# Optimization experiments

Measured on AMD Instinct MI355X. Metric: run time of the kernel, lower is better.

Reference implementation:

```python
import jax, jax.numpy as jnp
import numpy as np

SEQ, BATCH, EMBED = 2048, 4, 768
NUM_HEADS = 12
HEAD_DIM = EMBED // NUM_HEADS
SCALING = HEAD_DIM ** -0.5


def setup_inputs() -> dict:
    key = jax.random.key(0)
    ks = jax.random.split(key, 9)
    std = 0.02
    d = {"x": jax.random.normal(ks[0], (SEQ, BATCH, EMBED), dtype=jnp.float32)}
    for i, n in enumerate(["q", "k", "v", "out"]):
        d[f"W{n}"] = jax.random.normal(ks[1 + 2 * i], (EMBED, EMBED), dtype=jnp.float32) * std
        d[f"b{n}"] = jax.random.normal(ks[2 + 2 * i], (EMBED,), dtype=jnp.float32) * std
    return d


def reference(x, Wq, bq, Wk, bk, Wv, bv, Wout, bout):
    # x: [tgt_len, bsz, embed_dim] (fairseq seq-first layout per forward body)
    T, B, E = x.shape
    H, Dh = NUM_HEADS, HEAD_DIM

    q = (x @ Wq.T + bq) * SCALING          # [T, B, E]
    k = x @ Wk.T + bk
    v = x @ Wv.T + bv

    # view(T, B*H, Dh).transpose(0, 1) -> [B*H, T, Dh]
    q = q.reshape(T, B * H, Dh).transpose(1, 0, 2)
    k = k.reshape(T, B * H, Dh).transpose(1, 0, 2)
    v = v.reshape(T, B * H, Dh).transpose(1, 0, 2)

    # bmm: [B*H, T, T] attention scores (full O(T^2) matrix, as in the original)
    scores = jnp.einsum('bqd,bkd->bqk', q, k)
    # util_softmax with onnx_trace=True: softmax in float32, then cast back
    probs = jax.nn.softmax(scores.astype(jnp.float32), axis=-1).astype(scores.dtype)
    # dropout p=0.0 -> identity

    attn = jnp.einsum('bqk,bkd->bqd', probs, v)           # [B*H, T, Dh]
    attn = attn.transpose(1, 0, 2).reshape(T, B, E)       # [T, B, E]
    return attn @ Wout.T + bout
```

## Files before the change

kernel.cpp:

```cpp
#include <hip/hip_runtime.h>
#include <hip/hip_bf16.h>

#define SEQ 2048
#define BATCH 4
#define EMBED 768
#define NHEAD 12
#define HDIM 64
#define NROWS (SEQ*BATCH)
#define GH (BATCH*NHEAD)
#define KVBLK 64
#define KVHALF (SEQ/2)

typedef __bf16 bf16;
typedef __attribute__((ext_vector_type(4))) __bf16 bf16x4;
typedef __attribute__((ext_vector_type(8))) __bf16 bf16x8;
typedef __attribute__((ext_vector_type(4))) float f32x4;

#define LOG2E 1.44269504088896340736f

__global__ __launch_bounds__(256) void cvt_kernel(const float* __restrict__ in,
                                                  bf16* __restrict__ out, int n4) {
  int i = blockIdx.x * 256 + threadIdx.x;
  if (i >= n4) return;
  float4 v = reinterpret_cast<const float4*>(in)[i];
  bf16x4 o;
  o[0] = (bf16)v.x; o[1] = (bf16)v.y; o[2] = (bf16)v.z; o[3] = (bf16)v.w;
  reinterpret_cast<bf16x4*>(out)[i] = o;
}

__global__ __launch_bounds__(256) void cvt_w4(const float* __restrict__ Wq,
                                              const float* __restrict__ Wk,
                                              const float* __restrict__ Wv,
                                              const float* __restrict__ Wo,
                                              bf16* __restrict__ Wqkvb,
                                              bf16* __restrict__ Wob) {
  const int n4 = EMBED * EMBED / 4;
  int i = blockIdx.x * 256 + threadIdx.x;
  if (i >= n4) return;
  const float* src;
  bf16* dst;
  switch (blockIdx.y) {
    case 0: src = Wq; dst = Wqkvb; break;
    case 1: src = Wk; dst = Wqkvb + EMBED * EMBED; break;
    case 2: src = Wv; dst = Wqkvb + 2 * EMBED * EMBED; break;
    default: src = Wo; dst = Wob; break;
  }
  float4 v = reinterpret_cast<const float4*>(src)[i];
  bf16x4 o;
  o[0] = (bf16)v.x; o[1] = (bf16)v.y; o[2] = (bf16)v.z; o[3] = (bf16)v.w;
  reinterpret_cast<bf16x4*>(dst)[i] = o;
}

__global__ __launch_bounds__(256) void gemm_qkv(const bf16* __restrict__ A,
                                                const bf16* __restrict__ B,
                                                const float* __restrict__ bq,
                                                const float* __restrict__ bk,
                                                const float* __restrict__ bv,
                                                bf16* __restrict__ Qh,
                                                bf16* __restrict__ Kh,
                                                bf16* __restrict__ Vt) {
  constexpr int K = EMBED;
  __shared__ bf16 As[128 * 32];
  __shared__ bf16 Bs[128 * 32];
  const int tid = threadIdx.x;
  const int l = tid & 63;
  const int w = tid >> 6;
  const int row0 = blockIdx.x * 128;
  const int col0 = blockIdx.y * 128;
  const int wm = (w >> 1) * 64;
  const int wn = (w & 1) * 64;
  const int l15 = l & 15, l4 = l >> 4;

  f32x4 acc[4][4] = {};

  for (int k0 = 0; k0 < K; k0 += 32) {
#pragma unroll
    for (int i = 0; i < 2; ++i) {
      int c = tid + i * 256;
      int r = c >> 2, cc = c & 3;
      __builtin_amdgcn_global_load_lds(
          (const __attribute__((address_space(1))) void*)(A + (size_t)(row0 + r) * K + k0 + cc * 8),
          (__attribute__((address_space(3))) void*)(As + c * 8), 16, 0, 0);
    }
#pragma unroll
    for (int i = 0; i < 2; ++i) {
      int c = tid + i * 256;
      int r = c >> 2, cc = c & 3;
      __builtin_amdgcn_global_load_lds(
          (const __attribute__((address_space(1))) void*)(B + (size_t)(col0 + r) * K + k0 + cc * 8),
          (__attribute__((address_space(3))) void*)(Bs + c * 8), 16, 0, 0);
    }
    __syncthreads();

    bf16x8 af[4], bfr[4];
#pragma unroll
    for (int i = 0; i < 4; ++i)
      af[i] = *reinterpret_cast<const bf16x8*>(&As[(wm + i * 16 + l15) * 32 + l4 * 8]);
#pragma unroll
    for (int j = 0; j < 4; ++j)
      bfr[j] = *reinterpret_cast<const bf16x8*>(&Bs[(wn + j * 16 + l15) * 32 + l4 * 8]);
#pragma unroll
    for (int i = 0; i < 4; ++i)
#pragma unroll
      for (int j = 0; j < 4; ++j)
        acc[i][j] = __builtin_amdgcn_mfma_f32_16x16x32_bf16(af[i], bfr[j], acc[i][j], 0, 0, 0);
    __syncthreads();
  }

  const int sel = blockIdx.y / 6;
  const float* bias = sel == 0 ? bq : (sel == 1 ? bk : bv);
  const int colbase = col0 - sel * EMBED;
#pragma unroll
  for (int i = 0; i < 4; ++i) {
#pragma unroll
    for (int j = 0; j < 4; ++j) {
      int col = colbase + wn + j * 16 + l15;
      float bia = bias[col];
#pragma unroll
      for (int r = 0; r < 4; ++r) {
        int row = row0 + wm + i * 16 + l4 * 4 + r;
        float v = acc[i][j][r] + bia;
        int t = row >> 2, bb = row & 3;
        int hh = col >> 6, d = col & 63;
        int g = bb * NHEAD + hh;
        if (sel == 0)      Qh[((size_t)g * SEQ + t) * HDIM + d] = (bf16)(v * (0.125f * LOG2E));
        else if (sel == 1) Kh[((size_t)g * SEQ + t) * HDIM + d] = (bf16)v;
        else               Vt[((size_t)g * HDIM + d) * SEQ + t] = (bf16)v;
      }
    }
  }
}

__global__ __launch_bounds__(256) void gemm_out(const bf16* __restrict__ A,
                                                const bf16* __restrict__ B,
                                                const float* __restrict__ bias,
                                                float* __restrict__ outp) {
  constexpr int K = EMBED;
  __shared__ bf16 As[128 * 32];
  __shared__ bf16 Bs[128 * 32];
  const int tid = threadIdx.x;
  const int l = tid & 63;
  const int w = tid >> 6;
  const int row0 = blockIdx.x * 128;
  const int col0 = blockIdx.y * 128;
  const int wm = (w >> 1) * 64;
  const int wn = (w & 1) * 64;
  const int l15 = l & 15, l4 = l >> 4;

  f32x4 acc[4][4] = {};

  for (int k0 = 0; k0 < K; k0 += 32) {
#pragma unroll
    for (int i = 0; i < 2; ++i) {
      int c = tid + i * 256;
      int r = c >> 2, cc = c & 3;
      __builtin_amdgcn_global_load_lds(
          (const __attribute__((address_space(1))) void*)(A + (size_t)(row0 + r) * K + k0 + cc * 8),
          (__attribute__((address_space(3))) void*)(As + c * 8), 16, 0, 0);
    }
#pragma unroll
    for (int i = 0; i < 2; ++i) {
      int c = tid + i * 256;
      int r = c >> 2, cc = c & 3;
      __builtin_amdgcn_global_load_lds(
          (const __attribute__((address_space(1))) void*)(B + (size_t)(col0 + r) * K + k0 + cc * 8),
          (__attribute__((address_space(3))) void*)(Bs + c * 8), 16, 0, 0);
    }
    __syncthreads();

    bf16x8 af[4], bfr[4];
#pragma unroll
    for (int i = 0; i < 4; ++i)
      af[i] = *reinterpret_cast<const bf16x8*>(&As[(wm + i * 16 + l15) * 32 + l4 * 8]);
#pragma unroll
    for (int j = 0; j < 4; ++j)
      bfr[j] = *reinterpret_cast<const bf16x8*>(&Bs[(wn + j * 16 + l15) * 32 + l4 * 8]);
#pragma unroll
    for (int i = 0; i < 4; ++i)
#pragma unroll
      for (int j = 0; j < 4; ++j)
        acc[i][j] = __builtin_amdgcn_mfma_f32_16x16x32_bf16(af[i], bfr[j], acc[i][j], 0, 0, 0);
    __syncthreads();
  }

#pragma unroll
  for (int i = 0; i < 4; ++i) {
#pragma unroll
    for (int j = 0; j < 4; ++j) {
      int col = col0 + wn + j * 16 + l15;
      float bia = bias[col];
#pragma unroll
      for (int r = 0; r < 4; ++r) {
        int row = row0 + wm + i * 16 + l4 * 4 + r;
        outp[(size_t)row * EMBED + col] = acc[i][j][r] + bia;
      }
    }
  }
}

__global__ __launch_bounds__(256, 4) void attn_kernel(const bf16* __restrict__ Qh,
                                                      const bf16* __restrict__ Kh,
                                                      const bf16* __restrict__ Vt,
                                                      bf16* __restrict__ O0,
                                                      bf16* __restrict__ O1,
                                                      float* __restrict__ Sums) {
  const int g = blockIdx.x % GH;
  const int r2 = blockIdx.x / GH;
  const int half = r2 & 1;
  const int q0 = (r2 >> 1) * 128;
  const int kvbase = half * KVHALF;
  const int tid = threadIdx.x;
  const int w = tid >> 6, l = tid & 63;
  const int l15 = l & 15, l4 = l >> 4;
  const int qw = q0 + w * 32;

  __shared__ bf16 Ks[2][KVBLK * HDIM];
  __shared__ bf16 Vs[HDIM * KVBLK];
  __shared__ bf16 P_all[4][32 * 64];

  bf16* P = (bf16*)P_all[w];
  const bf16* Qp = Qh + (size_t)g * SEQ * HDIM;
  const bf16* Kp = Kh + (size_t)g * SEQ * HDIM;
  const bf16* Vp = Vt + (size_t)g * HDIM * SEQ;

#define STAGE_K(buf, kv0)                                                               \
  do {                                                                                  \
    _Pragma("unroll") for (int i = 0; i < 2; ++i) {                                     \
      int t = i * 256 + tid;                                                            \
      int r = t >> 3, c = t & 7;                                                        \
      __builtin_amdgcn_global_load_lds(                                                 \
          (const __attribute__((address_space(1))) void*)(Kp + (size_t)((kv0) + r) * HDIM + ((c ^ (r & 7)) * 8)), \
          (__attribute__((address_space(3))) void*)(&Ks[buf][t * 8]), 16, 0, 0);        \
    }                                                                                   \
  } while (0)

#define STAGE_V(kv0)                                                                    \
  do {                                                                                  \
    _Pragma("unroll") for (int i = 0; i < 2; ++i) {                                     \
      int t = i * 256 + tid;                                                            \
      int r = t >> 3, c = t & 7;                                                        \
      __builtin_amdgcn_global_load_lds(                                                 \
          (const __attribute__((address_space(1))) void*)(Vp + (size_t)r * SEQ + (kv0) + ((c ^ (r & 7)) * 8)), \
          (__attribute__((address_space(3))) void*)(&Vs[t * 8]), 16, 0, 0);             \
    }                                                                                   \
  } while (0)

  bf16x8 aq[2][2];
#pragma unroll
  for (int qf = 0; qf < 2; ++qf)
#pragma unroll
    for (int ks = 0; ks < 2; ++ks)
      aq[qf][ks] = *reinterpret_cast<const bf16x8*>(
          Qp + (size_t)(qw + qf * 16 + l15) * HDIM + ks * 32 + l4 * 8);

  bf16x8 vone;
#pragma unroll
  for (int i = 0; i < 8; ++i) vone[i] = (bf16)1.0f;

  f32x4 acco[2][4] = {};
  f32x4 accs[2] = {};

  STAGE_K(0, kvbase);
  __syncthreads();

  int cur = 0;
  for (int kv0 = kvbase; kv0 < kvbase + KVHALF; kv0 += KVBLK) {
    STAGE_V(kv0);
    STAGE_K(cur ^ 1, kvbase + (((kv0 - kvbase) + KVBLK) & (KVHALF - 1)));

    f32x4 s[2][4] = {};
#pragma unroll
    for (int kf = 0; kf < 4; ++kf) {
      int row = kf * 16 + l15;
#pragma unroll
      for (int ks = 0; ks < 2; ++ks) {
        bf16x8 bk = *reinterpret_cast<const bf16x8*>(
            &Ks[cur][row * 64 + (((ks * 4 + l4) ^ (row & 7)) * 8)]);
        __builtin_amdgcn_s_setprio(1);
        s[0][kf] = __builtin_amdgcn_mfma_f32_16x16x32_bf16(bk, aq[0][ks], s[0][kf], 0, 0, 0);
        s[1][kf] = __builtin_amdgcn_mfma_f32_16x16x32_bf16(bk, aq[1][ks], s[1][kf], 0, 0, 0);
        __builtin_amdgcn_s_setprio(0);
      }
    }

#pragma unroll
    for (int qf = 0; qf < 2; ++qf) {
      int prow = qf * 16 + l15;
#pragma unroll
      for (int kf = 0; kf < 4; ++kf) {
        float p0 = exp2f(s[qf][kf][0]);
        float p1 = exp2f(s[qf][kf][1]);
        float p2 = exp2f(s[qf][kf][2]);
        float p3 = exp2f(s[qf][kf][3]);
        bf16x4 pk;
        pk[0] = (bf16)p0; pk[1] = (bf16)p1; pk[2] = (bf16)p2; pk[3] = (bf16)p3;
        int chunk = (2 * kf + (l4 >> 1)) ^ (prow & 7);
        *reinterpret_cast<bf16x4*>(&P[prow * 64 + chunk * 8 + (l4 & 1) * 4]) = pk;
      }
    }

    asm volatile("s_waitcnt vmcnt(2)" ::: "memory");

#pragma unroll
    for (int ks = 0; ks < 2; ++ks) {
      bf16x8 ap[2];
#pragma unroll
      for (int qf = 0; qf < 2; ++qf) {
        int prow = qf * 16 + l15;
        int lc = ks * 4 + l4;
        ap[qf] = *reinterpret_cast<const bf16x8*>(P + prow * 64 + ((lc ^ (prow & 7)) << 3));
      }
#pragma unroll
      for (int df = 0; df < 4; ++df) {
        int row = df * 16 + l15;
        bf16x8 bv = *reinterpret_cast<const bf16x8*>(
            &Vs[row * 64 + (((ks * 4 + l4) ^ (row & 7)) * 8)]);
        __builtin_amdgcn_s_setprio(1);
        acco[0][df] = __builtin_amdgcn_mfma_f32_16x16x32_bf16(ap[0], bv, acco[0][df], 0, 0, 0);
        acco[1][df] = __builtin_amdgcn_mfma_f32_16x16x32_bf16(ap[1], bv, acco[1][df], 0, 0, 0);
        __builtin_amdgcn_s_setprio(0);
      }
      __builtin_amdgcn_s_setprio(1);
      accs[0] = __builtin_amdgcn_mfma_f32_16x16x32_bf16(ap[0], vone, accs[0], 0, 0, 0);
      accs[1] = __builtin_amdgcn_mfma_f32_16x16x32_bf16(ap[1], vone, accs[1], 0, 0, 0);
      __builtin_amdgcn_s_setprio(0);
    }
    __syncthreads();
    cur ^= 1;
  }

  bf16* Op = half ? O1 : O0;
  float* Sp = Sums + (size_t)half * GH * SEQ + (size_t)g * SEQ;
  const int bb = g / NHEAD, hh = g % NHEAD;
#pragma unroll
  for (int qf = 0; qf < 2; ++qf)
#pragma unroll
    for (int r = 0; r < 4; ++r) {
      int tq = qw + qf * 16 + l4 * 4 + r;
      if (l15 == 0) Sp[tq] = accs[qf][r];
#pragma unroll
      for (int df = 0; df < 4; ++df) {
        int d = df * 16 + l15;
        Op[((size_t)tq * BATCH + bb) * EMBED + hh * HDIM + d] = (bf16)acco[qf][df][r];
      }
    }
}

__global__ __launch_bounds__(256) void attn_combine(const bf16* __restrict__ O0,
                                                    const bf16* __restrict__ O1,
                                                    const float* __restrict__ Sums,
                                                    bf16* __restrict__ attnb) {
  int i = blockIdx.x * 256 + threadIdx.x;
  int flat = i * 8;
  int row = flat / EMBED;
  int e = flat - row * EMBED;
  int tq = row >> 2, bb = row & 3;
  int hh = e >> 6;
  int g = bb * NHEAD + hh;
  float s = Sums[(size_t)g * SEQ + tq] + Sums[(size_t)GH * SEQ + (size_t)g * SEQ + tq];
  float rinv = __builtin_amdgcn_rcpf(s);
  bf16x8 a0 = *reinterpret_cast<const bf16x8*>(O0 + flat);
  bf16x8 a1 = *reinterpret_cast<const bf16x8*>(O1 + flat);
  bf16x8 o;
#pragma unroll
  for (int j = 0; j < 8; ++j)
    o[j] = (bf16)(((float)a0[j] + (float)a1[j]) * rinv);
  *reinterpret_cast<bf16x8*>(attnb + flat) = o;
}

extern "C" void kernel_launch(void* const* d_in, const int* in_sizes, int n_in,
                              void* d_out, int out_size, void* d_ws, size_t ws_size,
                              hipStream_t stream) {
  const float* x  = (const float*)d_in[0];
  const float* Wq = (const float*)d_in[1];
  const float* bq = (const float*)d_in[2];
  const float* Wk = (const float*)d_in[3];
  const float* bk = (const float*)d_in[4];
  const float* Wv = (const float*)d_in[5];
  const float* bv = (const float*)d_in[6];
  const float* Wo = (const float*)d_in[7];
  const float* bo = (const float*)d_in[8];
  float* out = (float*)d_out;

  char* ws = (char*)d_ws;
  bf16* xb    = (bf16*)(ws + 0);
  bf16* Wqkvb = (bf16*)(ws + 12582912);
  bf16* Wob   = (bf16*)(ws + 16121856);
  bf16* Qh    = (bf16*)(ws + 17301504);
  bf16* Kh    = (bf16*)(ws + 29884416);
  bf16* Vt    = (bf16*)(ws + 42467328);
  bf16* attnb = (bf16*)(ws + 55050240);
  float* Sums = (float*)(ws + 67633152);

  cvt_kernel<<<6144, 256, 0, stream>>>(x, xb, NROWS * EMBED / 4);
  cvt_w4<<<dim3(576, 4), 256, 0, stream>>>(Wq, Wk, Wv, Wo, Wqkvb, Wob);

  gemm_qkv<<<dim3(NROWS / 128, 18), 256, 0, stream>>>(xb, Wqkvb, bq, bk, bv, Qh, Kh, Vt);

  attn_kernel<<<GH * (SEQ / 128) * 2, 256, 0, stream>>>(Qh, Kh, Vt, xb, attnb, Sums);
  attn_combine<<<NROWS * EMBED / 8 / 256, 256, 0, stream>>>(xb, attnb, Sums, attnb);

  gemm_out<<<dim3(NROWS / 128, EMBED / 128), 256, 0, stream>>>(attnb, Wob, bo, out);
}
```

Before: 172.5 us.

## Rewrite attention inner loop with 32x32 MFMA and register-resident P

The attention kernel moves from 16x16x32 to 32x32x16 bf16 MFMAs and computes transposed scores (K as A operand), so the exponentiated probabilities stay in registers. They are rearranged with cross-half-wave shuffles instead of round-tripping through shared memory. The row sum is accumulated in fp32 scalar adds rather than an extra MFMA against a ones vector. V is also double-buffered in LDS alongside K, which removes the mid-iteration vmcnt wait. The cost is more shuffles and selects and a larger LDS footprint for V, with the P buffer removed.

```diff
diff --git a/kernel.cpp b/kernel.cpp
--- a/kernel.cpp
+++ b/kernel.cpp
@@ -15,6 +15,9 @@
 typedef __attribute__((ext_vector_type(4))) __bf16 bf16x4;
 typedef __attribute__((ext_vector_type(8))) __bf16 bf16x8;
 typedef __attribute__((ext_vector_type(4))) float f32x4;
+typedef __attribute__((ext_vector_type(16))) float f32x16;
+typedef __attribute__((ext_vector_type(2))) unsigned uint2v;
+typedef __attribute__((ext_vector_type(4))) unsigned uint4v;
 
 #define LOG2E 1.44269504088896340736f
 
@@ -211,14 +214,13 @@
   const int kvbase = half * KVHALF;
   const int tid = threadIdx.x;
   const int w = tid >> 6, l = tid & 63;
-  const int l15 = l & 15, l4 = l >> 4;
+  const int l31 = l & 31, l5 = l >> 5;
   const int qw = q0 + w * 32;
+  const int r7 = l31 & 7;
 
   __shared__ bf16 Ks[2][KVBLK * HDIM];
-  __shared__ bf16 Vs[HDIM * KVBLK];
-  __shared__ bf16 P_all[4][32 * 64];
-
-  bf16* P = (bf16*)P_all[w];
+  __shared__ bf16 Vs[2][HDIM * KVBLK];
+
   const bf16* Qp = Qh + (size_t)g * SEQ * HDIM;
   const bf16* Kp = Kh + (size_t)g * SEQ * HDIM;
   const bf16* Vp = Vt + (size_t)g * HDIM * SEQ;
@@ -227,122 +229,114 @@
   do {                                                                                  \
     _Pragma("unroll") for (int i = 0; i < 2; ++i) {                                     \
       int t = i * 256 + tid;                                                            \
-      int r = t >> 3, c = t & 7;                                                        \
+      int r_ = t >> 3, c_ = t & 7;                                                      \
       __builtin_amdgcn_global_load_lds(                                                 \
-          (const __attribute__((address_space(1))) void*)(Kp + (size_t)((kv0) + r) * HDIM + ((c ^ (r & 7)) * 8)), \
+          (const __attribute__((address_space(1))) void*)(Kp + (size_t)((kv0) + r_) * HDIM + ((c_ ^ (r_ & 7)) * 8)), \
           (__attribute__((address_space(3))) void*)(&Ks[buf][t * 8]), 16, 0, 0);        \
     }                                                                                   \
   } while (0)
 
-#define STAGE_V(kv0)                                                                    \
+#define STAGE_V(buf, kv0)                                                               \
   do {                                                                                  \
     _Pragma("unroll") for (int i = 0; i < 2; ++i) {                                     \
       int t = i * 256 + tid;                                                            \
-      int r = t >> 3, c = t & 7;                                                        \
+      int r_ = t >> 3, c_ = t & 7;                                                      \
       __builtin_amdgcn_global_load_lds(                                                 \
-          (const __attribute__((address_space(1))) void*)(Vp + (size_t)r * SEQ + (kv0) + ((c ^ (r & 7)) * 8)), \
-          (__attribute__((address_space(3))) void*)(&Vs[t * 8]), 16, 0, 0);             \
+          (const __attribute__((address_space(1))) void*)(Vp + (size_t)r_ * SEQ + (kv0) + ((c_ ^ (r_ & 7)) * 8)), \
+          (__attribute__((address_space(3))) void*)(&Vs[buf][t * 8]), 16, 0, 0);        \
     }                                                                                   \
   } while (0)
 
-  bf16x8 aq[2][2];
-#pragma unroll
-  for (int qf = 0; qf < 2; ++qf)
-#pragma unroll
-    for (int ks = 0; ks < 2; ++ks)
-      aq[qf][ks] = *reinterpret_cast<const bf16x8*>(
-          Qp + (size_t)(qw + qf * 16 + l15) * HDIM + ks * 32 + l4 * 8);
-
-  bf16x8 vone;
-#pragma unroll
-  for (int i = 0; i < 8; ++i) vone[i] = (bf16)1.0f;
-
-  f32x4 acco[2][4] = {};
-  f32x4 accs[2] = {};
+  bf16x8 bq[4];
+#pragma unroll
+  for (int m = 0; m < 4; ++m)
+    bq[m] = *reinterpret_cast<const bf16x8*>(
+        Qp + (size_t)(qw + l31) * HDIM + m * 16 + l5 * 8);
+
+  f32x16 acco[2] = {};
+  float lsum = 0.f;
 
   STAGE_K(0, kvbase);
+  STAGE_V(0, kvbase);
   __syncthreads();
 
   int cur = 0;
   for (int kv0 = kvbase; kv0 < kvbase + KVHALF; kv0 += KVBLK) {
-    STAGE_V(kv0);
-    STAGE_K(cur ^ 1, kvbase + (((kv0 - kvbase) + KVBLK) & (KVHALF - 1)));
-
-    f32x4 s[2][4] = {};
-#pragma unroll
-    for (int kf = 0; kf < 4; ++kf) {
-      int row = kf * 16 + l15;
-#pragma unroll
-      for (int ks = 0; ks < 2; ++ks) {
-        bf16x8 bk = *reinterpret_cast<const bf16x8*>(
-            &Ks[cur][row * 64 + (((ks * 4 + l4) ^ (row & 7)) * 8)]);
+    int nxt = kvbase + (((kv0 - kvbase) + KVBLK) & (KVHALF - 1));
+    STAGE_V(cur ^ 1, nxt);
+    STAGE_K(cur ^ 1, nxt);
+
+#pragma unroll
+    for (int h = 0; h < 2; ++h) {
+      f32x16 s = {};
+#pragma unroll
+      for (int m = 0; m < 4; ++m) {
+        bf16x8 ak = *reinterpret_cast<const bf16x8*>(
+            &Ks[cur][(32 * h + l31) * 64 + (((2 * m + l5) ^ r7) * 8)]);
         __builtin_amdgcn_s_setprio(1);
-        s[0][kf] = __builtin_amdgcn_mfma_f32_16x16x32_bf16(bk, aq[0][ks], s[0][kf], 0, 0, 0);
-        s[1][kf] = __builtin_amdgcn_mfma_f32_16x16x32_bf16(bk, aq[1][ks], s[1][kf], 0, 0, 0);
+        s = __builtin_amdgcn_mfma_f32_32x32x16_bf16(ak, bq[m], s, 0, 0, 0);
         __builtin_amdgcn_s_setprio(0);
       }
-    }
-
-#pragma unroll
-    for (int qf = 0; qf < 2; ++qf) {
-      int prow = qf * 16 + l15;
-#pragma unroll
-      for (int kf = 0; kf < 4; ++kf) {
-        float p0 = exp2f(s[qf][kf][0]);
-        float p1 = exp2f(s[qf][kf][1]);
-        float p2 = exp2f(s[qf][kf][2]);
-        float p3 = exp2f(s[qf][kf][3]);
-        bf16x4 pk;
-        pk[0] = (bf16)p0; pk[1] = (bf16)p1; pk[2] = (bf16)p2; pk[3] = (bf16)p3;
-        int chunk = (2 * kf + (l4 >> 1)) ^ (prow & 7);
-        *reinterpret_cast<bf16x4*>(&P[prow * 64 + chunk * 8 + (l4 & 1) * 4]) = pk;
-      }
-    }
-
-    asm volatile("s_waitcnt vmcnt(2)" ::: "memory");
-
-#pragma unroll
-    for (int ks = 0; ks < 2; ++ks) {
-      bf16x8 ap[2];
-#pragma unroll
-      for (int qf = 0; qf < 2; ++qf) {
-        int prow = qf * 16 + l15;
-        int lc = ks * 4 + l4;
-        ap[qf] = *reinterpret_cast<const bf16x8*>(P + prow * 64 + ((lc ^ (prow & 7)) << 3));
-      }
-#pragma unroll
-      for (int df = 0; df < 4; ++df) {
-        int row = df * 16 + l15;
-        bf16x8 bv = *reinterpret_cast<const bf16x8*>(
-            &Vs[row * 64 + (((ks * 4 + l4) ^ (row & 7)) * 8)]);
-        __builtin_amdgcn_s_setprio(1);
-        acco[0][df] = __builtin_amdgcn_mfma_f32_16x16x32_bf16(ap[0], bv, acco[0][df], 0, 0, 0);
-        acco[1][df] = __builtin_amdgcn_mfma_f32_16x16x32_bf16(ap[1], bv, acco[1][df], 0, 0, 0);
-        __builtin_amdgcn_s_setprio(0);
-      }
-      __builtin_amdgcn_s_setprio(1);
-      accs[0] = __builtin_amdgcn_mfma_f32_16x16x32_bf16(ap[0], vone, accs[0], 0, 0, 0);
-      accs[1] = __builtin_amdgcn_mfma_f32_16x16x32_bf16(ap[1], vone, accs[1], 0, 0, 0);
-      __builtin_amdgcn_s_setprio(0);
+
+      unsigned pg[8];
+#pragma unroll
+      for (int gq = 0; gq < 4; ++gq) {
+        float p0 = exp2f(s[4 * gq + 0]);
+        float p1 = exp2f(s[4 * gq + 1]);
+        float p2 = exp2f(s[4 * gq + 2]);
+        float p3 = exp2f(s[4 * gq + 3]);
+        lsum += (p0 + p1) + (p2 + p3);
+        bf16x4 q4;
+        q4[0] = (bf16)p0; q4[1] = (bf16)p1; q4[2] = (bf16)p2; q4[3] = (bf16)p3;
+        uint2v d2 = __builtin_bit_cast(uint2v, q4);
+        pg[2 * gq] = d2[0];
+        pg[2 * gq + 1] = d2[1];
+      }
+
+#pragma unroll
+      for (int j = 0; j < 2; ++j) {
+        unsigned sx = l5 ? pg[4 * j + 0] : pg[4 * j + 2];
+        unsigned sy = l5 ? pg[4 * j + 1] : pg[4 * j + 3];
+        unsigned rx = (unsigned)__shfl_xor((int)sx, 32);
+        unsigned ry = (unsigned)__shfl_xor((int)sy, 32);
+        unsigned ox = l5 ? pg[4 * j + 2] : pg[4 * j + 0];
+        unsigned oy = l5 ? pg[4 * j + 3] : pg[4 * j + 1];
+        uint4v f;
+        f[0] = l5 ? rx : ox;  f[1] = l5 ? ry : oy;
+        f[2] = l5 ? ox : rx;  f[3] = l5 ? oy : ry;
+        bf16x8 pb = __builtin_bit_cast(bf16x8, f);
+#pragma unroll
+        for (int dt = 0; dt < 2; ++dt) {
+          bf16x8 av = *reinterpret_cast<const bf16x8*>(
+              &Vs[cur][(dt * 32 + l31) * 64 + (((4 * h + 2 * j + l5) ^ r7) * 8)]);
+          __builtin_amdgcn_s_setprio(1);
+          acco[dt] = __builtin_amdgcn_mfma_f32_32x32x16_bf16(av, pb, acco[dt], 0, 0, 0);
+          __builtin_amdgcn_s_setprio(0);
+        }
+      }
     }
     __syncthreads();
     cur ^= 1;
   }
 
+  float tot = lsum + __shfl_xor(lsum, 32);
   bf16* Op = half ? O1 : O0;
   float* Sp = Sums + (size_t)half * GH * SEQ + (size_t)g * SEQ;
+  const int tq = qw + l31;
+  if (l5 == 0) Sp[tq] = tot;
   const int bb = g / NHEAD, hh = g % NHEAD;
-#pragma unroll
-  for (int qf = 0; qf < 2; ++qf)
-#pragma unroll
-    for (int r = 0; r < 4; ++r) {
-      int tq = qw + qf * 16 + l4 * 4 + r;
-      if (l15 == 0) Sp[tq] = accs[qf][r];
-#pragma unroll
-      for (int df = 0; df < 4; ++df) {
-        int d = df * 16 + l15;
-        Op[((size_t)tq * BATCH + bb) * EMBED + hh * HDIM + d] = (bf16)acco[qf][df][r];
-      }
+  const size_t rowbase = ((size_t)tq * BATCH + bb) * EMBED + hh * HDIM;
+#pragma unroll
+  for (int dt = 0; dt < 2; ++dt)
+#pragma unroll
+    for (int gq = 0; gq < 4; ++gq) {
+      int d = dt * 32 + 8 * gq + 4 * l5;
+      bf16x4 o4;
+      o4[0] = (bf16)acco[dt][4 * gq + 0];
+      o4[1] = (bf16)acco[dt][4 * gq + 1];
+      o4[2] = (bf16)acco[dt][4 * gq + 2];
+      o4[3] = (bf16)acco[dt][4 * gq + 3];
+      *reinterpret_cast<bf16x4*>(Op + rowbase + d) = o4;
     }
 }
 
```

After: 180.8 us. +4.8%, slower.
